# Kernel optimization log

Measured on AMD Instinct MI355X. Metric: run time of the kernel, lower is better.

Reference implementation:

```python
import jax, jax.numpy as jnp
import numpy as np

B = 65536      # batch size
H = 256        # hidden_size (args['hid_dim'])
MID = 300      # hard-coded encoder bottleneck in CommonFeatureExtractor
THR = 0.6      # similarity_threshold


def _lin(k, fin, fout):
    return jax.random.normal(k, (fin, fout), jnp.float32) / np.sqrt(fin)


def setup_inputs() -> dict:
    key = jax.random.key(0)
    ks = jax.random.split(key, 24)
    inp = {
        'brics': jax.random.normal(ks[0], (B, H), jnp.float32),
        'function_group': jax.random.normal(ks[1], (B, H), jnp.float32),
        'pharmacophore': jax.random.normal(ks[2], (B, H), jnp.float32),
    }
    # three fp encoders: Linear(H,300) -> ReLU -> (Dropout eval) -> Linear(300,H)
    for n, (k1, k2) in zip(['b', 'f', 'p'], [(ks[3], ks[4]), (ks[5], ks[6]), (ks[7], ks[8])]):
        inp['W1_' + n] = _lin(k1, H, MID)
        inp['b1_' + n] = jnp.zeros((MID,), jnp.float32)
        inp['W2_' + n] = _lin(k2, MID, H)
        inp['b2_' + n] = jnp.zeros((H,), jnp.float32)
    inp['Wg'] = _lin(ks[9], 3 * H, 3)        # weight_generator
    inp['bg_v'] = jnp.zeros((3,), jnp.float32)
    inp['We'] = _lin(ks[10], H, H)           # enhancement_layer
    inp['be_v'] = jnp.zeros((H,), jnp.float32)
    inp['Wf'] = _lin(ks[11], 2 * H, H)       # fusion_layer
    inp['bf_v'] = jnp.zeros((H,), jnp.float32)
    return inp


def _fwd(brics, function_group, pharmacophore,
         W1_b, b1_b, W2_b, b2_b, W1_f, b1_f, W2_f, b2_f, W1_p, b1_p, W2_p, b2_p,
         Wg, bg_v, We, be_v, Wf, bf_v):
    def enc(x, W1, b1, W2, b2):
        return jax.nn.relu(x @ W1 + b1) @ W2 + b2  # dropout in eval mode = identity

    eb = enc(brics, W1_b, b1_b, W2_b, b2_b)
    ef = enc(function_group, W1_f, b1_f, W2_f, b2_f)
    ep = enc(pharmacophore, W1_p, b1_p, W2_p, b2_p)

    fps = jnp.stack([eb, ef, ep], axis=1)                              # [B,3,H]
    fpn = fps / jnp.maximum(jnp.linalg.norm(fps, axis=-1, keepdims=True), 1e-12)

    # the 3 unordered pairs (0,1),(0,2),(1,2); the torch sort is irrelevant
    # because the selected pairs are combined by a permutation-invariant
    # softmax-weighted sum.
    ii = jnp.array([0, 0, 1])
    jj = jnp.array([1, 2, 2])
    elem = fpn[:, ii] * fpn[:, jj]                                     # [B,3,H]
    sims = elem.sum(-1)                                                # [B,3] cosine sims
    pmask = sims > THR
    common = 0.5 * (fps[:, ii] + fps[:, jj]) * (elem > THR)            # [B,3,H]

    has = pmask.any(-1)                                                # [B]
    m = jnp.max(jnp.where(pmask, sims, -jnp.inf), axis=-1, keepdims=True)
    m = jnp.where(jnp.isfinite(m), m, 0.0)
    e = jnp.where(pmask, jnp.exp(sims - m), 0.0)                       # masked softmax
    w = e / jnp.maximum(e.sum(-1, keepdims=True), 1e-12)
    sample_common = (common * w[..., None]).sum(1)                     # [B,H]
    common_features = jnp.where(has[:, None], sample_common, fps.mean(1))

    allc = jnp.concatenate([eb, ef, ep], axis=1)                       # [B,3H]
    fw = jax.nn.softmax(allc @ Wg + bg_v, axis=1)                      # [B,3]
    weighted = eb * fw[:, 0:1] + ef * fw[:, 1:2] + ep * fw[:, 2:3]

    enh = jax.nn.sigmoid(common_features @ We + be_v)
    fused = jnp.concatenate([weighted, common_features * enh], axis=1) @ Wf + bf_v
    return fused


def reference(brics, function_group, pharmacophore,
              W1_b, b1_b, W2_b, b2_b, W1_f, b1_f, W2_f, b2_f, W1_p, b1_p, W2_p, b2_p,
              Wg, bg_v, We, be_v, Wf, bf_v):
    return _fwd(brics, function_group, pharmacophore,
                W1_b, b1_b, W2_b, b2_b, W1_f, b1_f, W2_f, b2_f, W1_p, b1_p, W2_p, b2_p,
                Wg, bg_v, We, be_v, Wf, bf_v)
```

## Files before the change

kernel.cpp:

```cpp
#include <hip/hip_runtime.h>

typedef unsigned short u16;
typedef __bf16 bf16x8 __attribute__((ext_vector_type(8)));
typedef float f32x4 __attribute__((ext_vector_type(4)));

__device__ __forceinline__ float b2f(u16 b){ union{unsigned u; float f;} v; v.u=((unsigned)b)<<16; return v.f; }
__device__ __forceinline__ u16 f2b(float f){ unsigned u=__builtin_bit_cast(unsigned,f); return (u16)((u+0x7fffu+((u>>16)&1u))>>16); }
__device__ __forceinline__ float wred(float v){
  #pragma unroll
  for(int off=32; off>0; off>>=1) v += __shfl_xor(v, off, 64);
  return v;
}
__device__ __forceinline__ void stOut(u16* p, float v){ *p = f2b(v); }
__device__ __forceinline__ void stOut(float* p, float v){ *p = v; }

__device__ __forceinline__ void gload_lds16(const void* g, void* l){
  __builtin_amdgcn_global_load_lds(
      (const __attribute__((address_space(1))) void*)g,
      (__attribute__((address_space(3))) void*)l, 16, 0, 0);
}

__device__ __forceinline__ void stageA8(u16* dst, const float* src){
  float4 a = *(const float4*)src;
  float4 b = *(const float4*)(src+4);
  ushort4 o0; o0.x=f2b(a.x); o0.y=f2b(a.y); o0.z=f2b(a.z); o0.w=f2b(a.w);
  ushort4 o1; o1.x=f2b(b.x); o1.y=f2b(b.y); o1.z=f2b(b.z); o1.w=f2b(b.w);
  *(ushort4*)dst = o0;
  *(ushort4*)(dst+4) = o1;
}

template<int MODE, typename OT, typename AT, bool DUAL>
__global__ __launch_bounds__(256) void gemm_k(
    const AT* __restrict__ A, const AT* __restrict__ A2, int lda,
    const u16* __restrict__ Wt, int K,
    const float* __restrict__ bias, int Nreal,
    OT* __restrict__ C, int ldc,
    const u16* __restrict__ mult, int ldm)
{
  __shared__ __align__(16) u16 As[128*64];
  __shared__ __align__(16) u16 Bs[64*64];
  const int tid = threadIdx.x;
  const size_t m0 = (size_t)blockIdx.x * 128;
  const int n0 = blockIdx.y * 64;
  const int lane = tid & 63, w = tid >> 6;
  const int lr = lane & 15, quad = lane >> 4;
  const int wr = (w >> 1) * 64, wc = (w & 1) * 32;
  const int swz = (lr & 7) << 3;
  const int KH = K >> 1;

  f32x4 acc[4][2];
  #pragma unroll
  for(int i=0;i<4;++i)
    #pragma unroll
    for(int j=0;j<2;++j) acc[i][j] = (f32x4){0.f,0.f,0.f,0.f};

  for(int k0=0; k0<K; k0+=64){
    const AT* Ap = A;
    int kcol = k0;
    if (DUAL && k0 >= KH) { Ap = A2; kcol = k0 - KH; }

    if constexpr (__is_same(AT, u16)) {
      #pragma unroll
      for(int it=0; it<4; ++it){
        int cbase = it*256 + w*64;
        int ch = cbase + lane;
        int r = ch >> 3;
        int ce = ((ch & 7) * 8) ^ ((r & 7) << 3);
        gload_lds16(Ap + (m0+r)*(size_t)lda + kcol + ce, &As[cbase*8]);
      }
    } else {
      #pragma unroll
      for(int it=0; it<4; ++it){
        int ch = tid + 256*it; int r = ch>>3, s = (ch&7)*8;
        stageA8(&As[r*64 + (s ^ ((r&7)<<3))], Ap + (m0+r)*(size_t)lda + kcol + s);
      }
    }
    #pragma unroll
    for(int it=0; it<2; ++it){
      int cbase = it*256 + w*64;
      int ch = cbase + lane;
      int r = ch >> 3;
      int ce = ((ch & 7) * 8) ^ ((r & 7) << 3);
      gload_lds16(Wt + (size_t)(n0+r)*K + k0 + ce, &Bs[cbase*8]);
    }
    __syncthreads();
    #pragma unroll
    for(int kk=0; kk<64; kk+=32){
      bf16x8 af[4], bfr[2];
      #pragma unroll
      for(int i=0;i<4;++i)
        af[i]  = *(const bf16x8*)&As[(wr + i*16 + lr)*64 + ((kk + quad*8) ^ swz)];
      #pragma unroll
      for(int j=0;j<2;++j)
        bfr[j] = *(const bf16x8*)&Bs[(wc + j*16 + lr)*64 + ((kk + quad*8) ^ swz)];
      #pragma unroll
      for(int i=0;i<4;++i)
        #pragma unroll
        for(int j=0;j<2;++j)
          acc[i][j] = __builtin_amdgcn_mfma_f32_16x16x32_bf16(af[i], bfr[j], acc[i][j], 0, 0, 0);
    }
    __syncthreads();
  }
  #pragma unroll
  for(int j=0;j<2;++j){
    int col = n0 + wc + j*16 + lr;
    float bv = (col < Nreal) ? bias[col] : 0.f;
    #pragma unroll
    for(int i=0;i<4;++i){
      #pragma unroll
      for(int r=0;r<4;++r){
        size_t row = m0 + wr + i*16 + quad*4 + r;
        size_t ci = row*(size_t)ldc + col;
        float v = acc[i][j][r] + bv;
        if(MODE==1) v = fmaxf(v, 0.f);
        if(MODE==2){
          float mv = b2f(mult[row*(size_t)ldm + col]);
          v = mv * __builtin_amdgcn_rcpf(1.f + __expf(-v));
        }
        stOut(&C[ci], v);
      }
    }
  }
}

struct TPar { const float* src; u16* dst; int K, N, Kp, Np; };
struct TArgs { TPar p[8]; };
__global__ __launch_bounds__(256) void transpose_all(TArgs args){
  TPar p = args.p[blockIdx.y];
  int n = blockIdx.x;
  if (n >= p.Np) return;
  for (int k = threadIdx.x; k < p.Kp; k += 256){
    u16 v = 0;
    if (n < p.N && k < p.K) v = f2b(p.src[(size_t)k*p.N + n]);
    p.dst[(size_t)n*p.Kp + k] = v;
  }
}

__global__ __launch_bounds__(256) void mid_k(
    const u16* eb, const u16* ef, const u16* ep,
    const float* __restrict__ Wg, const float* __restrict__ bg,
    u16* common, u16* weighted)
{
  const int wid = threadIdx.x >> 6, lane = threadIdx.x & 63;
  const size_t row = (size_t)blockIdx.x * 4 + wid;
  const size_t base = row*256 + lane*4;

  ushort4 vb = *(const ushort4*)(eb + base);
  ushort4 vf = *(const ushort4*)(ef + base);
  ushort4 vp = *(const ushort4*)(ep + base);
  float fb[4] = {b2f(vb.x), b2f(vb.y), b2f(vb.z), b2f(vb.w)};
  float ff[4] = {b2f(vf.x), b2f(vf.y), b2f(vf.z), b2f(vf.w)};
  float fp[4] = {b2f(vp.x), b2f(vp.y), b2f(vp.z), b2f(vp.w)};

  float sb=0, sf=0, sp=0, d01=0, d02=0, d12=0, g0=0, g1=0, g2=0;
  #pragma unroll
  for(int j=0;j<4;++j){
    sb += fb[j]*fb[j]; sf += ff[j]*ff[j]; sp += fp[j]*fp[j];
    d01 += fb[j]*ff[j]; d02 += fb[j]*fp[j]; d12 += ff[j]*fp[j];
  }
  #pragma unroll
  for(int seg=0; seg<3; ++seg){
    const float* x = (seg==0) ? fb : (seg==1) ? ff : fp;
    const float* wg = Wg + ((size_t)seg*256 + lane*4)*3;
    float4 w0 = *(const float4*)(wg);
    float4 w1 = *(const float4*)(wg+4);
    float4 w2 = *(const float4*)(wg+8);
    float wv[12] = {w0.x,w0.y,w0.z,w0.w, w1.x,w1.y,w1.z,w1.w, w2.x,w2.y,w2.z,w2.w};
    #pragma unroll
    for(int j=0;j<4;++j){
      g0 += x[j]*wv[j*3+0];
      g1 += x[j]*wv[j*3+1];
      g2 += x[j]*wv[j*3+2];
    }
  }
  sb=wred(sb); sf=wred(sf); sp=wred(sp);
  d01=wred(d01); d02=wred(d02); d12=wred(d12);
  g0=wred(g0); g1=wred(g1); g2=wred(g2);

  float inb  = __builtin_amdgcn_rsqf(fmaxf(sb, 1e-24f));
  float invf = __builtin_amdgcn_rsqf(fmaxf(sf, 1e-24f));
  float inp  = __builtin_amdgcn_rsqf(fmaxf(sp, 1e-24f));
  float s01 = d01*inb*invf, s02 = d02*inb*inp, s12 = d12*invf*inp;

  g0 += bg[0]; g1 += bg[1]; g2 += bg[2];
  float gm = fmaxf(g0, fmaxf(g1, g2));
  float e0 = __expf(g0-gm), e1 = __expf(g1-gm), e2 = __expf(g2-gm);
  float res = __builtin_amdgcn_rcpf(e0+e1+e2);
  float fw0 = e0*res, fw1 = e1*res, fw2 = e2*res;

  bool p0 = s01 > 0.6f, p1 = s02 > 0.6f, p2 = s12 > 0.6f;
  bool has = p0 || p1 || p2;
  float mm = -__builtin_inff();
  if(p0) mm = fmaxf(mm, s01);
  if(p1) mm = fmaxf(mm, s02);
  if(p2) mm = fmaxf(mm, s12);
  if(!has) mm = 0.f;
  float q0 = p0 ? __expf(s01-mm) : 0.f;
  float q1 = p1 ? __expf(s02-mm) : 0.f;
  float q2 = p2 ? __expf(s12-mm) : 0.f;
  float rqs = __builtin_amdgcn_rcpf(fmaxf(q0+q1+q2, 1e-12f));
  float w0 = q0*rqs, w1 = q1*rqs, w2 = q2*rqs;

  u16 co[4], wt[4];
  #pragma unroll
  for(int j=0;j<4;++j){
    float a = fb[j], b = ff[j], c = fp[j];
    float na = a*inb, nbv = b*invf, nc = c*inp;
    float c0 = (na*nbv > 0.6f) ? 0.5f*(a+b) : 0.f;
    float c1 = (na*nc  > 0.6f) ? 0.5f*(a+c) : 0.f;
    float c2 = (nbv*nc > 0.6f) ? 0.5f*(b+c) : 0.f;
    float sc = c0*w0 + c1*w1 + c2*w2;
    float cf = has ? sc : (a+b+c)*(1.f/3.f);
    float wv = a*fw0 + b*fw1 + c*fw2;
    co[j] = f2b(cf); wt[j] = f2b(wv);
  }
  ushort4 oc, ow;
  oc.x=co[0]; oc.y=co[1]; oc.z=co[2]; oc.w=co[3];
  ow.x=wt[0]; ow.y=wt[1]; ow.z=wt[2]; ow.w=wt[3];
  *(ushort4*)(common + base) = oc;
  *(ushort4*)(weighted + base) = ow;
}

extern "C" void kernel_launch(void* const* d_in, const int* in_sizes, int n_in,
                              void* d_out, int out_size, void* d_ws, size_t ws_size,
                              hipStream_t stream) {
  const float* brics = (const float*)d_in[0];
  const float* fg    = (const float*)d_in[1];
  const float* ph    = (const float*)d_in[2];
  const float* W1[3] = {(const float*)d_in[3], (const float*)d_in[7], (const float*)d_in[11]};
  const float* b1[3] = {(const float*)d_in[4], (const float*)d_in[8], (const float*)d_in[12]};
  const float* W2[3] = {(const float*)d_in[5], (const float*)d_in[9], (const float*)d_in[13]};
  const float* b2[3] = {(const float*)d_in[6], (const float*)d_in[10], (const float*)d_in[14]};
  const float* Wg = (const float*)d_in[15];
  const float* bg = (const float*)d_in[16];
  const float* We = (const float*)d_in[17];
  const float* be = (const float*)d_in[18];
  const float* Wf = (const float*)d_in[19];
  const float* bf = (const float*)d_in[20];
  float* out = (float*)d_out;

  const int M = in_sizes[0] / 256;

  char* wsp = (char*)d_ws;
  size_t off = 0;
  auto carve = [&](size_t elems)->u16* {
    u16* p = (u16*)(wsp + off);
    off += ((elems*sizeof(u16)) + 255) & ~(size_t)255;
    return p;
  };
  u16* xb0 = carve((size_t)M*256);
  u16* xb1 = carve((size_t)M*256);
  u16* xb2 = carve((size_t)M*256);
  u16* h   = carve((size_t)M*320);
  u16* Wt1[3], *Wt2[3];
  for(int i=0;i<3;++i) Wt1[i] = carve(320*256);
  for(int i=0;i<3;++i) Wt2[i] = carve(256*320);
  u16* WtE = carve(256*256);
  u16* WtF = carve(256*512);
  (void)ws_size; (void)n_in; (void)out_size;

  TArgs ta;
  for(int i=0;i<3;++i){
    ta.p[i]   = {W1[i], Wt1[i], 256, 300, 256, 320};
    ta.p[3+i] = {W2[i], Wt2[i], 300, 256, 320, 256};
  }
  ta.p[6] = {We, WtE, 256, 256, 256, 256};
  ta.p[7] = {Wf, WtF, 512, 256, 512, 256};
  transpose_all<<<dim3(512, 8), 256, 0, stream>>>(ta);

  const float* xin[3] = {brics, fg, ph};
  u16* encp[3] = {xb0, xb1, xb2};
  for(int i=0;i<3;++i){
    gemm_k<1,u16,float,false><<<dim3(M/128, 5), 256, 0, stream>>>(
        xin[i], nullptr, 256, Wt1[i], 256, b1[i], 300, h, 320, nullptr, 0);
    gemm_k<0,u16,u16,false><<<dim3(M/128, 4), 256, 0, stream>>>(
        h, nullptr, 320, Wt2[i], 320, b2[i], 256, encp[i], 256, nullptr, 0);
  }

  mid_k<<<M/4, 256, 0, stream>>>(xb0, xb1, xb2, Wg, bg, xb2, xb0);

  gemm_k<2,u16,u16,false><<<dim3(M/128, 4), 256, 0, stream>>>(
      xb2, nullptr, 256, WtE, 256, be, 256, xb1, 256, xb2, 256);

  gemm_k<0,float,u16,true><<<dim3(M/128, 4), 256, 0, stream>>>(
      xb0, xb1, 256, WtF, 512, bf, 256, out, 256, nullptr, 0);
}
```

Before: 522.9 us.

## Batch three encoder GEMMs per stage into one grid-z launch and widen mid_k

The three per-fingerprint encoder GEMM pairs are merged into two launches that use blockIdx.z to pick the encoder, with a separate hidden buffer for each encoder when the workspace allows. This removes four launches and the serialisation through a single shared hidden buffer, so the three encoders' blocks can fill the GPU together. mid_k now processes two rows per wavefront with 16-byte loads and 32-lane reductions. The cost is extra workspace for the three hidden buffers, with a fallback path when it is too small.

Result: no change. 530.2 us (+1.4%).

```diff
diff --git a/kernel.cpp b/kernel.cpp
--- a/kernel.cpp
+++ b/kernel.cpp
@@ -3,12 +3,13 @@
 typedef unsigned short u16;
 typedef __bf16 bf16x8 __attribute__((ext_vector_type(8)));
 typedef float f32x4 __attribute__((ext_vector_type(4)));
+typedef unsigned short u16x8 __attribute__((ext_vector_type(8)));
 
 __device__ __forceinline__ float b2f(u16 b){ union{unsigned u; float f;} v; v.u=((unsigned)b)<<16; return v.f; }
 __device__ __forceinline__ u16 f2b(float f){ unsigned u=__builtin_bit_cast(unsigned,f); return (u16)((u+0x7fffu+((u>>16)&1u))>>16); }
-__device__ __forceinline__ float wred(float v){
-  #pragma unroll
-  for(int off=32; off>0; off>>=1) v += __shfl_xor(v, off, 64);
+__device__ __forceinline__ float wred32(float v){
+  #pragma unroll
+  for(int off=16; off>0; off>>=1) v += __shfl_xor(v, off, 64);
   return v;
 }
 __device__ __forceinline__ void stOut(u16* p, float v){ *p = f2b(v); }
@@ -29,14 +30,27 @@
   *(ushort4*)(dst+4) = o1;
 }
 
+struct GP {
+  const void* A[3];
+  const void* A2;
+  const u16*  Wt[3];
+  const float* bias[3];
+  void* C[3];
+  const u16* mult;
+  int lda, K, Nreal, ldc, ldm;
+};
+
 template<int MODE, typename OT, typename AT, bool DUAL>
-__global__ __launch_bounds__(256) void gemm_k(
-    const AT* __restrict__ A, const AT* __restrict__ A2, int lda,
-    const u16* __restrict__ Wt, int K,
-    const float* __restrict__ bias, int Nreal,
-    OT* __restrict__ C, int ldc,
-    const u16* __restrict__ mult, int ldm)
+__global__ __launch_bounds__(256) void gemm_k(GP p)
 {
+  const int z = blockIdx.z;
+  const AT* __restrict__ A  = (const AT*)p.A[z];
+  const AT* __restrict__ A2 = (const AT*)p.A2;
+  const u16* __restrict__ Wt = p.Wt[z];
+  const float* __restrict__ bias = p.bias[z];
+  OT* __restrict__ C = (OT*)p.C[z];
+  const int lda = p.lda, K = p.K, Nreal = p.Nreal, ldc = p.ldc, ldm = p.ldm;
+
   __shared__ __align__(16) u16 As[128*64];
   __shared__ __align__(16) u16 Bs[64*64];
   const int tid = threadIdx.x;
@@ -114,7 +128,7 @@
         float v = acc[i][j][r] + bv;
         if(MODE==1) v = fmaxf(v, 0.f);
         if(MODE==2){
-          float mv = b2f(mult[row*(size_t)ldm + col]);
+          float mv = b2f(p.mult[row*(size_t)ldm + col]);
           v = mv * __builtin_amdgcn_rcpf(1.f + __expf(-v));
         }
         stOut(&C[ci], v);
@@ -142,40 +156,43 @@
     u16* common, u16* weighted)
 {
   const int wid = threadIdx.x >> 6, lane = threadIdx.x & 63;
-  const size_t row = (size_t)blockIdx.x * 4 + wid;
-  const size_t base = row*256 + lane*4;
-
-  ushort4 vb = *(const ushort4*)(eb + base);
-  ushort4 vf = *(const ushort4*)(ef + base);
-  ushort4 vp = *(const ushort4*)(ep + base);
-  float fb[4] = {b2f(vb.x), b2f(vb.y), b2f(vb.z), b2f(vb.w)};
-  float ff[4] = {b2f(vf.x), b2f(vf.y), b2f(vf.z), b2f(vf.w)};
-  float fp[4] = {b2f(vp.x), b2f(vp.y), b2f(vp.z), b2f(vp.w)};
+  const int half = lane >> 5, l5 = lane & 31;
+  const size_t row = (size_t)blockIdx.x * 8 + wid*2 + half;
+  const size_t base = row*256 + l5*8;
+
+  u16x8 vb = *(const u16x8*)(eb + base);
+  u16x8 vf = *(const u16x8*)(ef + base);
+  u16x8 vp = *(const u16x8*)(ep + base);
+  float fb[8], ff[8], fp[8];
+  #pragma unroll
+  for(int j=0;j<8;++j){ fb[j]=b2f(vb[j]); ff[j]=b2f(vf[j]); fp[j]=b2f(vp[j]); }
 
   float sb=0, sf=0, sp=0, d01=0, d02=0, d12=0, g0=0, g1=0, g2=0;
   #pragma unroll
-  for(int j=0;j<4;++j){
+  for(int j=0;j<8;++j){
     sb += fb[j]*fb[j]; sf += ff[j]*ff[j]; sp += fp[j]*fp[j];
     d01 += fb[j]*ff[j]; d02 += fb[j]*fp[j]; d12 += ff[j]*fp[j];
   }
   #pragma unroll
   for(int seg=0; seg<3; ++seg){
     const float* x = (seg==0) ? fb : (seg==1) ? ff : fp;
-    const float* wg = Wg + ((size_t)seg*256 + lane*4)*3;
-    float4 w0 = *(const float4*)(wg);
-    float4 w1 = *(const float4*)(wg+4);
-    float4 w2 = *(const float4*)(wg+8);
-    float wv[12] = {w0.x,w0.y,w0.z,w0.w, w1.x,w1.y,w1.z,w1.w, w2.x,w2.y,w2.z,w2.w};
-    #pragma unroll
-    for(int j=0;j<4;++j){
+    const float* wg = Wg + ((size_t)seg*256 + l5*8)*3;
+    float wv[24];
+    #pragma unroll
+    for(int q=0;q<6;++q){
+      float4 t = *(const float4*)(wg + q*4);
+      wv[q*4+0]=t.x; wv[q*4+1]=t.y; wv[q*4+2]=t.z; wv[q*4+3]=t.w;
+    }
+    #pragma unroll
+    for(int j=0;j<8;++j){
       g0 += x[j]*wv[j*3+0];
       g1 += x[j]*wv[j*3+1];
       g2 += x[j]*wv[j*3+2];
     }
   }
-  sb=wred(sb); sf=wred(sf); sp=wred(sp);
-  d01=wred(d01); d02=wred(d02); d12=wred(d12);
-  g0=wred(g0); g1=wred(g1); g2=wred(g2);
+  sb=wred32(sb); sf=wred32(sf); sp=wred32(sp);
+  d01=wred32(d01); d02=wred32(d02); d12=wred32(d12);
+  g0=wred32(g0); g1=wred32(g1); g2=wred32(g2);
 
   float inb  = __builtin_amdgcn_rsqf(fmaxf(sb, 1e-24f));
   float invf = __builtin_amdgcn_rsqf(fmaxf(sf, 1e-24f));
@@ -201,9 +218,9 @@
   float rqs = __builtin_amdgcn_rcpf(fmaxf(q0+q1+q2, 1e-12f));
   float w0 = q0*rqs, w1 = q1*rqs, w2 = q2*rqs;
 
-  u16 co[4], wt[4];
-  #pragma unroll
-  for(int j=0;j<4;++j){
+  u16x8 oc, ow;
+  #pragma unroll
+  for(int j=0;j<8;++j){
     float a = fb[j], b = ff[j], c = fp[j];
     float na = a*inb, nbv = b*invf, nc = c*inp;
     float c0 = (na*nbv > 0.6f) ? 0.5f*(a+b) : 0.f;
@@ -212,13 +229,10 @@
     float sc = c0*w0 + c1*w1 + c2*w2;
     float cf = has ? sc : (a+b+c)*(1.f/3.f);
     float wv = a*fw0 + b*fw1 + c*fw2;
-    co[j] = f2b(cf); wt[j] = f2b(wv);
-  }
-  ushort4 oc, ow;
-  oc.x=co[0]; oc.y=co[1]; oc.z=co[2]; oc.w=co[3];
-  ow.x=wt[0]; ow.y=wt[1]; ow.z=wt[2]; ow.w=wt[3];
-  *(ushort4*)(common + base) = oc;
-  *(ushort4*)(weighted + base) = ow;
+    oc[j] = f2b(cf); ow[j] = f2b(wv);
+  }
+  *(u16x8*)(common + base) = oc;
+  *(u16x8*)(weighted + base) = ow;
 }
 
 extern "C" void kernel_launch(void* const* d_in, const int* in_sizes, int n_in,
@@ -251,13 +265,19 @@
   u16* xb0 = carve((size_t)M*256);
   u16* xb1 = carve((size_t)M*256);
   u16* xb2 = carve((size_t)M*256);
-  u16* h   = carve((size_t)M*320);
   u16* Wt1[3], *Wt2[3];
   for(int i=0;i<3;++i) Wt1[i] = carve(320*256);
   for(int i=0;i<3;++i) Wt2[i] = carve(256*320);
   u16* WtE = carve(256*256);
   u16* WtF = carve(256*512);
-  (void)ws_size; (void)n_in; (void)out_size;
+
+  size_t hb = (((size_t)M*320*sizeof(u16)) + 255) & ~(size_t)255;
+  bool batched = (off + 3*hb) <= ws_size;
+  u16* hh[3];
+  hh[0] = (u16*)(wsp + off);
+  hh[1] = batched ? (u16*)(wsp + off + hb)   : hh[0];
+  hh[2] = batched ? (u16*)(wsp + off + 2*hb) : hh[0];
+  (void)n_in; (void)out_size;
 
   TArgs ta;
   for(int i=0;i<3;++i){
@@ -270,18 +290,37 @@
 
   const float* xin[3] = {brics, fg, ph};
   u16* encp[3] = {xb0, xb1, xb2};
-  for(int i=0;i<3;++i){
-    gemm_k<1,u16,float,false><<<dim3(M/128, 5), 256, 0, stream>>>(
-        xin[i], nullptr, 256, Wt1[i], 256, b1[i], 300, h, 320, nullptr, 0);
-    gemm_k<0,u16,u16,false><<<dim3(M/128, 4), 256, 0, stream>>>(
-        h, nullptr, 320, Wt2[i], 320, b2[i], 256, encp[i], 256, nullptr, 0);
-  }
-
-  mid_k<<<M/4, 256, 0, stream>>>(xb0, xb1, xb2, Wg, bg, xb2, xb0);
-
-  gemm_k<2,u16,u16,false><<<dim3(M/128, 4), 256, 0, stream>>>(
-      xb2, nullptr, 256, WtE, 256, be, 256, xb1, 256, xb2, 256);
-
-  gemm_k<0,float,u16,true><<<dim3(M/128, 4), 256, 0, stream>>>(
-      xb0, xb1, 256, WtF, 512, bf, 256, out, 256, nullptr, 0);
-}
+  if (batched) {
+    GP g1{};
+    for(int i=0;i<3;++i){ g1.A[i]=xin[i]; g1.Wt[i]=Wt1[i]; g1.bias[i]=b1[i]; g1.C[i]=hh[i]; }
+    g1.lda=256; g1.K=256; g1.Nreal=300; g1.ldc=320;
+    gemm_k<1,u16,float,false><<<dim3(M/128, 5, 3), 256, 0, stream>>>(g1);
+    GP g2{};
+    for(int i=0;i<3;++i){ g2.A[i]=hh[i]; g2.Wt[i]=Wt2[i]; g2.bias[i]=b2[i]; g2.C[i]=encp[i]; }
+    g2.lda=320; g2.K=320; g2.Nreal=256; g2.ldc=256;
+    gemm_k<0,u16,u16,false><<<dim3(M/128, 4, 3), 256, 0, stream>>>(g2);
+  } else {
+    for(int i=0;i<3;++i){
+      GP g1{}; g1.A[0]=xin[i]; g1.Wt[0]=Wt1[i]; g1.bias[0]=b1[i]; g1.C[0]=hh[0];
+      g1.lda=256; g1.K=256; g1.Nreal=300; g1.ldc=320;
+      gemm_k<1,u16,float,false><<<dim3(M/128, 5, 1), 256, 0, stream>>>(g1);
+      GP g2{}; g2.A[0]=hh[0]; g2.Wt[0]=Wt2[i]; g2.bias[0]=b2[i]; g2.C[0]=encp[i];
+      g2.lda=320; g2.K=320; g2.Nreal=256; g2.ldc=256;
+      gemm_k<0,u16,u16,false><<<dim3(M/128, 4, 1), 256, 0, stream>>>(g2);
+    }
+  }
+
+  mid_k<<<M/8, 256, 0, stream>>>(xb0, xb1, xb2, Wg, bg, xb2, xb0);
+
+  {
+    GP gg{}; gg.A[0]=xb2; gg.Wt[0]=WtE; gg.bias[0]=be; gg.C[0]=xb1;
+    gg.mult=xb2; gg.lda=256; gg.K=256; gg.Nreal=256; gg.ldc=256; gg.ldm=256;
+    gemm_k<2,u16,u16,false><<<dim3(M/128, 4, 1), 256, 0, stream>>>(gg);
+  }
+
+  {
+    GP gf{}; gf.A[0]=xb0; gf.A2=xb1; gf.Wt[0]=WtF; gf.bias[0]=bf; gf.C[0]=out;
+    gf.lda=256; gf.K=512; gf.Nreal=256; gf.ldc=256;
+    gemm_k<0,float,u16,true><<<dim3(M/128, 4, 1), 256, 0, stream>>>(gf);
+  }
+}
```
